# Kernel tuning notes

Hardware: AMD Instinct MI355X
Metric: run time of the kernel (lower is better)

Reference implementation:

```python
import jax, jax.numpy as jnp
import numpy as np

H = 1024   # hidden_size
A = 16     # num_actions
T = 64     # time steps
N = 128    # batch (parallel envs)


def setup_inputs() -> dict:
    key = jax.random.key(0)
    ks = jax.random.split(key, 16)
    s = 0.02  # small-ish init scale for weights
    a_idx = jax.random.randint(ks[5], (T, N), 0, A)
    return {
        "x": jax.random.normal(ks[0], (T * N, H), jnp.float32),
        "hxs_gru": jax.random.normal(ks[1], (N, H), jnp.float32),
        "hxs_p": jax.random.normal(ks[2], (N, 2 * H), jnp.float32),
        # masks are 0/1 episode-reset flags
        "masks": jax.random.bernoulli(ks[3], 0.95, (T * N, 1)).astype(jnp.float32),
        "prev_action_one_hot": jax.nn.one_hot(a_idx, A, dtype=jnp.float32),
        "w_ih": jax.random.normal(ks[6], (3 * H, H), jnp.float32) * s,
        "w_hh": jax.random.normal(ks[7], (3 * H, H), jnp.float32) * s,
        "b_ih": jnp.zeros((3 * H,), jnp.float32),
        "b_hh": jnp.zeros((3 * H,), jnp.float32),
        "p_w1": jax.random.normal(ks[8], (2 * H, 2 * H + A), jnp.float32) * s,
        "p_b1": jnp.zeros((2 * H,), jnp.float32),
        "p_w2": jax.random.normal(ks[9], (H, 2 * H), jnp.float32) * s,
        "p_b2": jnp.zeros((H,), jnp.float32),
        "mu_w": jax.random.normal(ks[10], (H, H), jnp.float32) * s,
        "mu_b": jnp.zeros((H,), jnp.float32),
        "lv_w": jax.random.normal(ks[11], (H, H), jnp.float32) * s,
        "lv_b": jnp.zeros((H,), jnp.float32),
    }


def reference(x, hxs_gru, hxs_p, masks, prev_action_one_hot,
              w_ih, w_hh, b_ih, b_hh,
              p_w1, p_b1, p_w2, p_b2,
              mu_w, mu_b, lv_w, lv_b):
    n = hxs_gru.shape[0]
    h_dim = hxs_gru.shape[1]
    t = x.shape[0] // n
    xT = x.reshape(t, n, h_dim)        # [T,N,H]
    mT = masks.reshape(t, n, 1)        # [T,N,1]

    # ---- _forward_gru: masked GRUCell recurrence over time ----
    def gru_step(h, inp):
        x_t, m_t = inp
        h0 = h * m_t                                  # per-step state reset
        gi = x_t @ w_ih.T + b_ih                      # [N,3H]
        gh = h0 @ w_hh.T + b_hh                       # [N,3H]
        ir, iz, inn = jnp.split(gi, 3, axis=1)
        hr, hz, hn = jnp.split(gh, 3, axis=1)
        r = jax.nn.sigmoid(ir + hr)
        z = jax.nn.sigmoid(iz + hz)
        nn_ = jnp.tanh(inn + r * hn)
        h_new = (1.0 - z) * nn_ + z * h0              # PyTorch GRUCell update
        return h_new, h_new

    gru_hxs, gru_acc = jax.lax.scan(gru_step, hxs_gru, (xT, mT))
    gru_acc = gru_acc.reshape(t * n, h_dim)

    # ---- _forward_p_gru: MLP recurrence with mask-gated state/action ----
    def p_step(h, inp):
        x_t, m_t, a_t = inp
        hidden = h * m_t + jnp.concatenate([x_t, x_t], axis=1) * (1.0 - m_t)
        cur = jnp.concatenate([a_t * m_t, hidden], axis=1)   # [N, A+2H]
        d = jax.nn.relu(cur @ p_w1.T + p_b1)                 # [N, 2H]
        d = jax.nn.relu(d @ p_w2.T + p_b2)                   # [N, H]
        mu = d @ mu_w.T + mu_b                               # [N, H]
        lv = d @ lv_w.T + lv_b                               # [N, H]
        h_new = jnp.concatenate([mu, x_t], axis=1)           # [N, 2H]
        return h_new, (mu, lv)

    # note: original concatenates action first: cat((a*m, hidden))
    p_hxs, (p_mu, p_lv) = jax.lax.scan(p_step, hxs_p, (xT, mT, prev_action_one_hot))
    p_mu = p_mu.reshape(t * n, h_dim)
    p_lv = p_lv.reshape(t * n, h_dim)
    return (gru_acc, gru_hxs, p_mu, p_lv, p_hxs)
```

## Files before the change

### kernel.cpp

```cpp
#include <hip/hip_runtime.h>

typedef unsigned int uint;
typedef unsigned short ushort;
typedef __bf16 bf16x8_t __attribute__((ext_vector_type(8)));
typedef float f32x4_t __attribute__((ext_vector_type(4)));
typedef uint u32x4_t __attribute__((ext_vector_type(4)));

__device__ __forceinline__ ushort f2b(float f) {
    uint u = __builtin_bit_cast(uint, f);
    u += 0x7fffu + ((u >> 16) & 1u);
    return (ushort)(u >> 16);
}
__device__ __forceinline__ float b2f(ushort h) {
    return __builtin_bit_cast(float, (uint)h << 16);
}
__device__ __forceinline__ float sigm(float v) { return 1.f / (1.f + __expf(-v)); }
__device__ __forceinline__ float tanh_(float v) {
    v = fmaxf(-15.f, fminf(15.f, v));
    float e = __expf(2.f * v);
    return (e - 1.f) / (e + 1.f);
}

__device__ __forceinline__ uint ld_cg_u32(const uint* p) {
    uint r;
    asm volatile("global_load_dword %0, %1, off sc0 sc1\n\ts_waitcnt vmcnt(0)"
                 : "=v"(r) : "v"(p) : "memory");
    return r;
}
__device__ __forceinline__ void st_cg_u32(uint* p, uint v) {
    asm volatile("global_store_dword %0, %1, off sc0 sc1" :: "v"(p), "v"(v) : "memory");
}
__device__ __forceinline__ void st_cg_u16(ushort* p, uint v) {
    asm volatile("global_store_short %0, %1, off sc0 sc1" :: "v"(p), "v"(v) : "memory");
}
__device__ __forceinline__ void st_cg_x4(ushort* p, u32x4_t v) {
    asm volatile("global_store_dwordx4 %0, %1, off sc0 sc1" :: "v"(p), "v"(v) : "memory");
}
__device__ __forceinline__ void ld8_nc(uint4 u[8],
    const void* p0, const void* p1, const void* p2, const void* p3,
    const void* p4, const void* p5, const void* p6, const void* p7)
{
    asm volatile(
        "global_load_dwordx4 %0, %8, off\n\t"
        "global_load_dwordx4 %1, %9, off\n\t"
        "global_load_dwordx4 %2, %10, off\n\t"
        "global_load_dwordx4 %3, %11, off\n\t"
        "global_load_dwordx4 %4, %12, off\n\t"
        "global_load_dwordx4 %5, %13, off\n\t"
        "global_load_dwordx4 %6, %14, off\n\t"
        "global_load_dwordx4 %7, %15, off"
        : "=&v"(u[0]), "=&v"(u[1]), "=&v"(u[2]), "=&v"(u[3]),
          "=&v"(u[4]), "=&v"(u[5]), "=&v"(u[6]), "=&v"(u[7])
        : "v"(p0), "v"(p1), "v"(p2), "v"(p3), "v"(p4), "v"(p5), "v"(p6), "v"(p7)
        : "memory");
}
__device__ __forceinline__ void vm0() {
    asm volatile("s_waitcnt vmcnt(0)" ::: "memory");
    __builtin_amdgcn_sched_barrier(0);
}
__device__ __forceinline__ bf16x8_t u2b(uint4 u) { return __builtin_bit_cast(bf16x8_t, u); }

#define SMEM_BYTES 36864
union U8 { ushort h[8]; uint4 v; };

template<int BN, int EPI, bool AF32>
__device__ __forceinline__ void gemm_body(
    int bx, int by, const void* Av, int lda,
    const ushort* Bp, int ldb, int K,
    void* Ov, int ldo, const float* bias, char* smem)
{
    constexpr int LDW = 72;
    ushort* As = (ushort*)smem;
    ushort* Bs = (ushort*)(smem + 128 * LDW * 2);
    const int tid = threadIdx.x, lane = tid & 63, wid = tid >> 6;
    constexpr int WC = (BN == 128) ? 2 : 1;
    constexpr int WR = 4 / WC;
    constexpr int WROWS = 128 / WR;
    constexpr int WCOLS = BN / WC;
    constexpr int MI = WROWS / 16, NI = WCOLS / 16;
    const int wr = (WC == 2) ? (wid >> 1) : wid;
    const int wc = (WC == 2) ? (wid & 1) : 0;
    const int row0 = by * 128, col0 = bx * BN;

    f32x4_t acc[MI][NI];
#pragma unroll
    for (int i = 0; i < MI; i++)
#pragma unroll
        for (int j = 0; j < NI; j++) acc[i][j] = (f32x4_t){0.f, 0.f, 0.f, 0.f};

    for (int k0 = 0; k0 < K; k0 += 64) {
        __syncthreads();
#pragma unroll
        for (int cc = 0; cc < 4; cc++) {
            int chunk = tid + cc * 256;
            int r = chunk >> 3, c8 = chunk & 7;
            uint4 val;
            if constexpr (AF32) {
                const float* Af = (const float*)Av + (size_t)(row0 + r) * lda + k0 + c8 * 8;
                float4 v0 = ((const float4*)Af)[0];
                float4 v1 = ((const float4*)Af)[1];
                U8 u;
                u.h[0] = f2b(v0.x); u.h[1] = f2b(v0.y); u.h[2] = f2b(v0.z); u.h[3] = f2b(v0.w);
                u.h[4] = f2b(v1.x); u.h[5] = f2b(v1.y); u.h[6] = f2b(v1.z); u.h[7] = f2b(v1.w);
                val = u.v;
            } else {
                val = *(const uint4*)((const ushort*)Av + (size_t)(row0 + r) * lda + k0 + c8 * 8);
            }
            *(uint4*)&As[r * LDW + c8 * 8] = val;
        }
#pragma unroll
        for (int cc = 0; cc < BN / 32; cc++) {
            int chunk = tid + cc * 256;
            int r = chunk >> 3, c8 = chunk & 7;
            uint4 val = *(const uint4*)(Bp + (size_t)(col0 + r) * ldb + k0 + c8 * 8);
            *(uint4*)&Bs[r * LDW + c8 * 8] = val;
        }
        __syncthreads();
#pragma unroll
        for (int kk = 0; kk < 64; kk += 32) {
            int ko = kk + ((lane >> 4) << 3);
            bf16x8_t af[MI], bf[NI];
#pragma unroll
            for (int mi = 0; mi < MI; mi++)
                af[mi] = *(const bf16x8_t*)&As[(wr * WROWS + mi * 16 + (lane & 15)) * LDW + ko];
#pragma unroll
            for (int ni = 0; ni < NI; ni++)
                bf[ni] = *(const bf16x8_t*)&Bs[(wc * WCOLS + ni * 16 + (lane & 15)) * LDW + ko];
#pragma unroll
            for (int mi = 0; mi < MI; mi++)
#pragma unroll
                for (int ni = 0; ni < NI; ni++)
                    acc[mi][ni] = __builtin_amdgcn_mfma_f32_16x16x32_bf16(af[mi], bf[ni], acc[mi][ni], 0, 0, 0);
        }
    }
#pragma unroll
    for (int mi = 0; mi < MI; mi++) {
#pragma unroll
        for (int ni = 0; ni < NI; ni++) {
            int gcol = col0 + wc * WCOLS + ni * 16 + (lane & 15);
#pragma unroll
            for (int i = 0; i < 4; i++) {
                int grow = row0 + wr * WROWS + mi * 16 + ((lane >> 4) << 2) + i;
                float v = acc[mi][ni][i];
                if constexpr (EPI == 0) {
                    ((float*)Ov)[(size_t)grow * ldo + gcol] = v + bias[gcol];
                } else if constexpr (EPI == 1) {
                    ((ushort*)Ov)[(size_t)grow * ldo + gcol] = f2b(v);
                } else if constexpr (EPI == 2) {
                    ((ushort*)Ov)[(size_t)grow * ldo + gcol] = f2b(v + bias[gcol]);
                } else if constexpr (EPI == 3) {
                    int t = grow >> 7, row = grow & 127;
                    int g = gcol >> 10, cb = (gcol & 1023) >> 4, c16 = gcol & 15;
                    ((ushort*)Ov)[(((size_t)t * 3 + g) * 64 + cb) * 2048 + row * 16 + c16] = f2b(v);
                } else {
                    int t = grow >> 7, row = grow & 127;
                    int cg = gcol >> 5, c32 = gcol & 31;
                    ((ushort*)Ov)[((size_t)t * 64 + cg) * 4096 + row * 32 + c32] = f2b(v + bias[gcol]);
                }
            }
        }
    }
}

template<int BN, int EPI, bool AF32>
__global__ __launch_bounds__(256) void gemm_k(
    const void* A, int lda, const ushort* B, int ldb, int K,
    void* O, int ldo, const float* bias)
{
    __shared__ char smem[SMEM_BYTES];
    gemm_body<BN, EPI, AF32>(blockIdx.x, blockIdx.y, A, lda, B, ldb, K, O, ldo, bias, smem);
}

__global__ __launch_bounds__(256) void gemm_rest_k(
    const void* A1, const ushort* B1, void* O1,
    const void* A2, const ushort* B2, void* O2,
    const float* p_w1, const float* mu_b, float* cvec)
{
    __shared__ char smem[SMEM_BYTES];
    int b = blockIdx.x;
    if (b < 1536) {
        gemm_body<128, 3, true>(b % 24, b / 24, A1, 1024, B1, 1024, 1024, O1, 0, nullptr, smem);
    } else if (b < 1664) {
        int c = b - 1536;
        gemm_body<128, 1, false>(c & 7, c >> 3, A2, 1024, B2, 1024, 1024, O2, 1024, nullptr, smem);
    } else {
        int j = (b - 1664) * 4 + (threadIdx.x >> 6);
        int lane = threadIdx.x & 63;
        float s = 0.f;
        for (int o = lane; o < 1024; o += 64) s += p_w1[(size_t)j * 2064 + 16 + o] * mu_b[o];
#pragma unroll
        for (int off = 32; off; off >>= 1) s += __shfl_down(s, off);
        if (lane == 0) cvec[j] = s;
    }
}

#define NFLAG_G 0
#define NFLAG_A 4096
#define NFLAG_B 12288
#define NFLAGS  20480

__device__ __forceinline__ void wv_wait16(uint* f, int lane) {
    if (lane < 16) {
        while (ld_cg_u32(f + lane) == 0u) {}
    }
    __builtin_amdgcn_sched_barrier(0);
}
__device__ __forceinline__ void wg_arrive(uint* slot, int tid) {
    __syncthreads();
    if (tid == 0) st_cg_u32(slot, 1u);
}

__device__ void role_gru(int cb, const ushort* __restrict__ whhb, ushort* hb,
                         const ushort* __restrict__ gi, const float* masks,
                         const float* b_ih, const float* b_hh, const float* hxs_g,
                         float* out, uint* flags, char* lds)
{
    const int tid = threadIdx.x, lane = tid & 63, w = tid >> 6;
    const int colL = cb * 16 + (lane & 15);
    const int kw = w * 256;
    const int kl = (lane >> 4) << 3;

    bf16x8_t bw[3][8];
#pragma unroll
    for (int g = 0; g < 3; g++)
#pragma unroll
        for (int ks = 0; ks < 8; ks++)
            bw[g][ks] = *(const bf16x8_t*)(whhb + (size_t)(g * 1024 + colL) * 1024 + kw + ks * 32 + kl);

    const float bihr = b_ih[colL], bihz = b_ih[1024 + colL], bihn = b_ih[2048 + colL];
    const float bhhr = b_hh[colL], bhhz = b_hh[1024 + colL], bhhn = b_hh[2048 + colL];

    f32x4_t hown[2];
#pragma unroll
    for (int j = 0; j < 2; j++)
#pragma unroll
        for (int i = 0; i < 4; i++)
            hown[j][i] = hxs_g[(size_t)((2 * w + j) * 16 + ((lane >> 4) << 2) + i) * 1024 + colL];

    for (int t = 0; t < 64; t++) {
        float mc[2][4], mn[2][4], g0p[2][4], g1p[2][4], g2p[2][4];
        const size_t gb = ((size_t)t * 3 * 64 + cb) * 2048;
#pragma unroll
        for (int j = 0; j < 2; j++) {
            const int rt = 2 * w + j;
#pragma unroll
            for (int i = 0; i < 4; i++) {
                const int row = rt * 16 + ((lane >> 4) << 2) + i;
                mc[j][i] = masks[t * 128 + row];
                mn[j][i] = (t < 63) ? masks[(t + 1) * 128 + row] : 0.f;
                g0p[j][i] = b2f(gi[gb + row * 16 + (lane & 15)]);
                g1p[j][i] = b2f(gi[gb + 131072 + row * 16 + (lane & 15)]);
                g2p[j][i] = b2f(gi[gb + 262144 + row * 16 + (lane & 15)]);
            }
        }
        if (t) wv_wait16(flags + NFLAG_G + (t - 1) * 64 + w * 16, lane);
        const ushort* base = hb + (size_t)t * 131072 + (size_t)(lane & 15) * 1024 + kw + kl;
        f32x4_t acc[3][8];
#pragma unroll
        for (int g = 0; g < 3; g++)
#pragma unroll
            for (int rt = 0; rt < 8; rt++) acc[g][rt] = (f32x4_t){0.f, 0.f, 0.f, 0.f};
#pragma unroll
        for (int half = 0; half < 2; half++) {
            const ushort* b = base + half * 128;
            uint4 u0[8], u1[8], u2[8], u3[8];
            ld8_nc(u0, b, b + 16384, b + 32768, b + 49152, b + 65536, b + 81920, b + 98304, b + 114688);
            ld8_nc(u1, b + 32, b + 16384 + 32, b + 32768 + 32, b + 49152 + 32, b + 65536 + 32, b + 81920 + 32, b + 98304 + 32, b + 114688 + 32);
            ld8_nc(u2, b + 64, b + 16384 + 64, b + 32768 + 64, b + 49152 + 64, b + 65536 + 64, b + 81920 + 64, b + 98304 + 64, b + 114688 + 64);
            ld8_nc(u3, b + 96, b + 16384 + 96, b + 32768 + 96, b + 49152 + 96, b + 65536 + 96, b + 81920 + 96, b + 98304 + 96, b + 114688 + 96);
            vm0();
#pragma unroll
            for (int g = 0; g < 3; g++)
#pragma unroll
                for (int rt = 0; rt < 8; rt++) {
                    acc[g][rt] = __builtin_amdgcn_mfma_f32_16x16x32_bf16(u2b(u0[rt]), bw[g][half * 4 + 0], acc[g][rt], 0, 0, 0);
                    acc[g][rt] = __builtin_amdgcn_mfma_f32_16x16x32_bf16(u2b(u1[rt]), bw[g][half * 4 + 1], acc[g][rt], 0, 0, 0);
                    acc[g][rt] = __builtin_amdgcn_mfma_f32_16x16x32_bf16(u2b(u2[rt]), bw[g][half * 4 + 2], acc[g][rt], 0, 0, 0);
                    acc[g][rt] = __builtin_amdgcn_mfma_f32_16x16x32_bf16(u2b(u3[rt]), bw[g][half * 4 + 3], acc[g][rt], 0, 0, 0);
                }
        }
        __syncthreads();
#pragma unroll
        for (int g = 0; g < 3; g++)
#pragma unroll
            for (int rt = 0; rt < 8; rt++)
                *(f32x4_t*)(lds + ((size_t)(w * 24 + g * 8 + rt) * 64 + lane) * 16) = acc[g][rt];
        __syncthreads();
#pragma unroll
        for (int j = 0; j < 2; j++) {
            const int rt = 2 * w + j;
            f32x4_t sg[3];
#pragma unroll
            for (int g = 0; g < 3; g++) {
                sg[g] = (f32x4_t){0.f, 0.f, 0.f, 0.f};
#pragma unroll
                for (int ww = 0; ww < 4; ww++)
                    sg[g] += *(const f32x4_t*)(lds + ((size_t)(ww * 24 + g * 8 + rt) * 64 + lane) * 16);
            }
#pragma unroll
            for (int i = 0; i < 4; i++) {
                const int row = rt * 16 + ((lane >> 4) << 2) + i;
                const float h0 = hown[j][i] * mc[j][i];
                const float rv = sigm(g0p[j][i] + bihr + bhhr + sg[0][i]);
                const float zv = sigm(g1p[j][i] + bihz + bhhz + sg[1][i]);
                const float nv = tanh_(g2p[j][i] + bihn + rv * (sg[2][i] + bhhn));
                const float hnew = (1.f - zv) * nv + zv * h0;
                out[(size_t)(t * 128 + row) * 1024 + colL] = hnew;
                hown[j][i] = hnew;
                if (t < 63)
                    st_cg_u16(hb + (size_t)(t + 1) * 131072 + (size_t)row * 1024 + colL,
                              (uint)f2b(hnew * mn[j][i]));
            }
        }
        wg_arrive(flags + NFLAG_G + t * 64 + cb, tid);
    }
}

__device__ void role_p(int p, const ushort* __restrict__ Wcb, const ushort* __restrict__ w1h1b,
                       const ushort* __restrict__ hp1b, const ushort* __restrict__ w2b,
                       const ushort* __restrict__ d1pre, const float* masks, const float* cvec,
                       const float* p_b2, ushort* d1r, ushort* d2r, uint* flags, char* lds)
{
    const int tid = threadIdx.x, lane = tid & 63, w = tid >> 6;
    const int rowg = p >> 6, colg = p & 63;
    const int rA0 = rowg * 64, cA0 = colg * 32;
    const int rB0 = rowg * 64, cB0 = colg * 16;
    const int kwA = w * 256, kwB = w * 512, kl = (lane >> 4) << 3;
    ushort* stg = (ushort*)(lds + 32768) + w * 512;

    bf16x8_t wcF[2][8];
#pragma unroll
    for (int ct = 0; ct < 2; ct++)
#pragma unroll
        for (int ks = 0; ks < 8; ks++)
            wcF[ct][ks] = *(const bf16x8_t*)(Wcb + (size_t)(cA0 + ct * 16 + (lane & 15)) * 1024 + kwA + ks * 32 + kl);
    bf16x8_t w2F[16];
#pragma unroll
    for (int ks = 0; ks < 16; ks++)
        w2F[ks] = *(const bf16x8_t*)(w2b + (size_t)(cB0 + (lane & 15)) * 2048 + kwB + ks * 32 + kl);
    const float cv0 = cvec[cA0 + (lane & 15)], cv1 = cvec[cA0 + 16 + (lane & 15)];
    const float pb = p_b2[cB0 + (lane & 15)];

    for (int t = 0; t < 64; t++) {
        float mA[4], preA[2][4];
        const size_t pbase = ((size_t)t * 64 + colg) * 4096;
#pragma unroll
        for (int i = 0; i < 4; i++) {
            const int row = rA0 + w * 16 + ((lane >> 4) << 2) + i;
            mA[i] = masks[t * 128 + row];
            preA[0][i] = b2f(d1pre[pbase + (row & 127) * 32 + (lane & 15)]);
            preA[1][i] = b2f(d1pre[pbase + (row & 127) * 32 + 16 + (lane & 15)]);
        }
        if (t) wv_wait16(flags + NFLAG_B + (t - 1) * 128 + rowg * 64 + w * 16, lane);
        f32x4_t accA[2][4];
#pragma unroll
        for (int ct = 0; ct < 2; ct++)
#pragma unroll
            for (int rt = 0; rt < 4; rt++) accA[ct][rt] = (f32x4_t){0.f, 0.f, 0.f, 0.f};
        if (t == 0) {
#pragma unroll
            for (int ks = 0; ks < 8; ks++) {
                bf16x8_t af[4], b0[2];
#pragma unroll
                for (int ct = 0; ct < 2; ct++)
                    b0[ct] = *(const bf16x8_t*)(w1h1b + (size_t)(cA0 + ct * 16 + (lane & 15)) * 1024 + kwA + ks * 32 + kl);
#pragma unroll
                for (int rt = 0; rt < 4; rt++)
                    af[rt] = *(const bf16x8_t*)(hp1b + (size_t)(rA0 + rt * 16 + (lane & 15)) * 1024 + kwA + ks * 32 + kl);
#pragma unroll
                for (int ct = 0; ct < 2; ct++)
#pragma unroll
                    for (int rt = 0; rt < 4; rt++)
                        accA[ct][rt] = __builtin_amdgcn_mfma_f32_16x16x32_bf16(af[rt], b0[ct], accA[ct][rt], 0, 0, 0);
            }
        } else {
            const ushort* Ab = d2r + (size_t)(t - 1) * 131072 + (size_t)(rA0 + (lane & 15)) * 1024 + kwA + kl;
            uint4 u0[8], u1[8], u2[8], u3[8];
            ld8_nc(u0, Ab,       Ab + 16384,       Ab + 32768,       Ab + 49152,       Ab + 32,  Ab + 16384 + 32,  Ab + 32768 + 32,  Ab + 49152 + 32);
            ld8_nc(u1, Ab + 64,  Ab + 16384 + 64,  Ab + 32768 + 64,  Ab + 49152 + 64,  Ab + 96,  Ab + 16384 + 96,  Ab + 32768 + 96,  Ab + 49152 + 96);
            ld8_nc(u2, Ab + 128, Ab + 16384 + 128, Ab + 32768 + 128, Ab + 49152 + 128, Ab + 160, Ab + 16384 + 160, Ab + 32768 + 160, Ab + 49152 + 160);
            ld8_nc(u3, Ab + 192, Ab + 16384 + 192, Ab + 32768 + 192, Ab + 49152 + 192, Ab + 224, Ab + 16384 + 224, Ab + 32768 + 224, Ab + 49152 + 224);
            vm0();
#pragma unroll
            for (int ct = 0; ct < 2; ct++)
#pragma unroll
                for (int rt = 0; rt < 4; rt++) {
                    accA[ct][rt] = __builtin_amdgcn_mfma_f32_16x16x32_bf16(u2b(u0[rt]), wcF[ct][0], accA[ct][rt], 0, 0, 0);
                    accA[ct][rt] = __builtin_amdgcn_mfma_f32_16x16x32_bf16(u2b(u0[4 + rt]), wcF[ct][1], accA[ct][rt], 0, 0, 0);
                    accA[ct][rt] = __builtin_amdgcn_mfma_f32_16x16x32_bf16(u2b(u1[rt]), wcF[ct][2], accA[ct][rt], 0, 0, 0);
                    accA[ct][rt] = __builtin_amdgcn_mfma_f32_16x16x32_bf16(u2b(u1[4 + rt]), wcF[ct][3], accA[ct][rt], 0, 0, 0);
                    accA[ct][rt] = __builtin_amdgcn_mfma_f32_16x16x32_bf16(u2b(u2[rt]), wcF[ct][4], accA[ct][rt], 0, 0, 0);
                    accA[ct][rt] = __builtin_amdgcn_mfma_f32_16x16x32_bf16(u2b(u2[4 + rt]), wcF[ct][5], accA[ct][rt], 0, 0, 0);
                    accA[ct][rt] = __builtin_amdgcn_mfma_f32_16x16x32_bf16(u2b(u3[rt]), wcF[ct][6], accA[ct][rt], 0, 0, 0);
                    accA[ct][rt] = __builtin_amdgcn_mfma_f32_16x16x32_bf16(u2b(u3[4 + rt]), wcF[ct][7], accA[ct][rt], 0, 0, 0);
                }
        }
        __syncthreads();
#pragma unroll
        for (int ct = 0; ct < 2; ct++)
#pragma unroll
            for (int rt = 0; rt < 4; rt++)
                *(f32x4_t*)(lds + ((size_t)(w * 8 + ct * 4 + rt) * 64 + lane) * 16) = accA[ct][rt];
        __syncthreads();
#pragma unroll
        for (int ct = 0; ct < 2; ct++) {
            f32x4_t s = (f32x4_t){0.f, 0.f, 0.f, 0.f};
#pragma unroll
            for (int ww = 0; ww < 4; ww++)
                s += *(const f32x4_t*)(lds + ((size_t)(ww * 8 + ct * 4 + w) * 64 + lane) * 16);
            const float cvt = (t == 0) ? 0.f : (ct ? cv1 : cv0);
#pragma unroll
            for (int i = 0; i < 4; i++) {
                float f = preA[ct][i] + mA[i] * (s[i] + cvt);
                stg[(((lane >> 4) << 2) + i) * 32 + ct * 16 + (lane & 15)] = f2b(f > 0.f ? f : 0.f);
            }
        }
        __syncthreads();
        {
            const int rl = lane >> 2, c8 = (lane & 3) * 8;
            u32x4_t v = *(const u32x4_t*)&stg[rl * 32 + c8];
            st_cg_x4(d1r + (size_t)t * 262144 + (size_t)(rA0 + w * 16 + rl) * 2048 + cA0 + c8, v);
        }
        wg_arrive(flags + NFLAG_A + t * 128 + p, tid);
        wv_wait16(flags + NFLAG_A + t * 128 + rowg * 64 + w * 16, lane);
        f32x4_t accB[4];
#pragma unroll
        for (int rt = 0; rt < 4; rt++) accB[rt] = (f32x4_t){0.f, 0.f, 0.f, 0.f};
        const ushort* Bb = d1r + (size_t)t * 262144 + (size_t)(rB0 + (lane & 15)) * 2048 + kwB + kl;
#pragma unroll
        for (int half = 0; half < 2; half++) {
            const ushort* b = Bb + half * 256;
            uint4 u0[8], u1[8], u2[8], u3[8];
            ld8_nc(u0, b,       b + 32768,       b + 65536,       b + 98304,       b + 32,  b + 32768 + 32,  b + 65536 + 32,  b + 98304 + 32);
            ld8_nc(u1, b + 64,  b + 32768 + 64,  b + 65536 + 64,  b + 98304 + 64,  b + 96,  b + 32768 + 96,  b + 65536 + 96,  b + 98304 + 96);
            ld8_nc(u2, b + 128, b + 32768 + 128, b + 65536 + 128, b + 98304 + 128, b + 160, b + 32768 + 160, b + 65536 + 160, b + 98304 + 160);
            ld8_nc(u3, b + 192, b + 32768 + 192, b + 65536 + 192, b + 98304 + 192, b + 224, b + 32768 + 224, b + 65536 + 224, b + 98304 + 224);
            vm0();
#pragma unroll
            for (int rt = 0; rt < 4; rt++) {
                accB[rt] = __builtin_amdgcn_mfma_f32_16x16x32_bf16(u2b(u0[rt]), w2F[half * 8 + 0], accB[rt], 0, 0, 0);
                accB[rt] = __builtin_amdgcn_mfma_f32_16x16x32_bf16(u2b(u0[4 + rt]), w2F[half * 8 + 1], accB[rt], 0, 0, 0);
                accB[rt] = __builtin_amdgcn_mfma_f32_16x16x32_bf16(u2b(u1[rt]), w2F[half * 8 + 2], accB[rt], 0, 0, 0);
                accB[rt] = __builtin_amdgcn_mfma_f32_16x16x32_bf16(u2b(u1[4 + rt]), w2F[half * 8 + 3], accB[rt], 0, 0, 0);
                accB[rt] = __builtin_amdgcn_mfma_f32_16x16x32_bf16(u2b(u2[rt]), w2F[half * 8 + 4], accB[rt], 0, 0, 0);
                accB[rt] = __builtin_amdgcn_mfma_f32_16x16x32_bf16(u2b(u2[4 + rt]), w2F[half * 8 + 5], accB[rt], 0, 0, 0);
                accB[rt] = __builtin_amdgcn_mfma_f32_16x16x32_bf16(u2b(u3[rt]), w2F[half * 8 + 6], accB[rt], 0, 0, 0);
                accB[rt] = __builtin_amdgcn_mfma_f32_16x16x32_bf16(u2b(u3[4 + rt]), w2F[half * 8 + 7], accB[rt], 0, 0, 0);
            }
        }
        __syncthreads();
#pragma unroll
        for (int rt = 0; rt < 4; rt++)
            *(f32x4_t*)(lds + ((size_t)(w * 4 + rt) * 64 + lane) * 16) = accB[rt];
        __syncthreads();
        {
            f32x4_t s = (f32x4_t){0.f, 0.f, 0.f, 0.f};
#pragma unroll
            for (int ww = 0; ww < 4; ww++)
                s += *(const f32x4_t*)(lds + ((size_t)(ww * 4 + w) * 64 + lane) * 16);
#pragma unroll
            for (int i = 0; i < 4; i++) {
                float f = s[i] + pb;
                stg[(((lane >> 4) << 2) + i) * 16 + (lane & 15)] = f2b(f > 0.f ? f : 0.f);
            }
        }
        __syncthreads();
        {
            if (lane < 32) {
                const int rl = lane >> 1, c8 = (lane & 1) * 8;
                u32x4_t v = *(const u32x4_t*)&stg[rl * 16 + c8];
                st_cg_x4(d2r + (size_t)t * 131072 + (size_t)(rB0 + w * 16 + rl) * 1024 + cB0 + c8, v);
            }
        }
        wg_arrive(flags + NFLAG_B + t * 128 + p, tid);
    }
}

__global__ __launch_bounds__(256, 1) void persist_k(
    const ushort* whhb, const ushort* Wcb, const ushort* w1h1b, const ushort* w2b,
    const ushort* gi, const ushort* d1pre, const ushort* hp1b,
    ushort* hb, ushort* d1r, ushort* d2r,
    const float* masks, const float* b_ih, const float* b_hh,
    const float* cvec, const float* p_b2, const float* hxs_g,
    float* out, uint* flags)
{
    __shared__ __align__(16) char lds[98304];
    const int wg = blockIdx.x;
    if (wg < 64) role_gru(wg, whhb, hb, gi, masks, b_ih, b_hh, hxs_g, out, flags, lds);
    else         role_p(wg - 64, Wcb, w1h1b, hp1b, w2b, d1pre, masks, cvec, p_b2, d1r, d2r, flags, lds);
}

__global__ void prep_all(const float* w_ih, const float* w_hh, const float* p_w1,
                         const float* p_w2, const float* mu_w, const float* lv_w,
                         const float* x, const float* hxs_g, const float* hxs_p,
                         const float* masks, const float* oh,
                         ushort* wihb, ushort* whhb, ushort* w2b, ushort* muwb,
                         ushort* lvwb, ushort* muwTb, ushort* w1h1b, ushort* pw1b,
                         ushort* ain, ushort* hb0, ushort* hp1b, uint* flags)
{
    const long totW = 17956864;
    const long totA = 8192L * 2112, totH = 131072, totP = 131072;
    const long total = totW + totA + totH + totP + NFLAGS;
    for (long idx = (long)blockIdx.x * 256 + threadIdx.x; idx < total; idx += (long)gridDim.x * 256) {
        long l = idx;
        if (l < 3145728) { wihb[l] = f2b(w_ih[l]); continue; } l -= 3145728;
        if (l < 3145728) { whhb[l] = f2b(w_hh[l]); continue; } l -= 3145728;
        if (l < 2097152) { w2b[l] = f2b(p_w2[l]); continue; } l -= 2097152;
        if (l < 1048576) { muwb[l] = f2b(mu_w[l]); continue; } l -= 1048576;
        if (l < 1048576) { lvwb[l] = f2b(lv_w[l]); continue; } l -= 1048576;
        if (l < 1048576) {
            int c = (int)(l >> 10), o = (int)(l & 1023);
            muwTb[l] = f2b(mu_w[(size_t)o * 1024 + c]); continue;
        } l -= 1048576;
        if (l < 2097152) {
            int r = (int)(l >> 10), c = (int)(l & 1023);
            w1h1b[l] = f2b(p_w1[(size_t)r * 2064 + 16 + c]); continue;
        } l -= 2097152;
        if (l < 4325376) {
            int r = (int)(l / 2112), c = (int)(l - (long)r * 2112);
            pw1b[l] = (c < 2064) ? f2b(p_w1[(size_t)r * 2064 + c]) : (ushort)0;
            continue;
        } l -= 4325376;
        if (l < totA) {
            int i = (int)(l / 2112);
            int c = (int)(l - (long)i * 2112);
            float m = masks[i];
            float v;
            if (c < 16) v = oh[(size_t)i * 16 + c] * m;
            else if (c < 1040) v = x[(size_t)i * 1024 + (c - 16)] * (1.f - m);
            else if (c < 2064) {
                int cc = c - 1040;
                float xp = (i >= 128) ? x[(size_t)(i - 128) * 1024 + cc]
                                      : hxs_p[(size_t)i * 2048 + 1024 + cc];
                v = xp * m + x[(size_t)i * 1024 + cc] * (1.f - m);
            } else v = 0.f;
            ain[l] = f2b(v);
            continue;
        } l -= totA;
        if (l < totH) {
            int row = (int)(l >> 10), c = (int)(l & 1023);
            hb0[l] = f2b(hxs_g[(size_t)row * 1024 + c] * masks[row]);
            continue;
        } l -= totH;
        if (l < totP) {
            int row = (int)(l >> 10), c = (int)(l & 1023);
            hp1b[l] = f2b(hxs_p[(size_t)row * 2048 + c]);
            continue;
        } l -= totP;
        flags[l] = 0u;
    }
}

__global__ void k_tail(float* out, const float* x)
{
    const long total = 131072 + 262144;
    for (long idx = (long)blockIdx.x * 256 + threadIdx.x; idx < total; idx += (long)gridDim.x * 256) {
        if (idx < 131072) {
            out[8388608 + idx] = out[8257536 + idx];
        } else {
            long j = idx - 131072;
            int n = (int)(j >> 11), c = (int)(j & 2047);
            out[25296896 + j] = (c < 1024)
                ? out[8519680 + (size_t)(8064 + n) * 1024 + c]
                : x[(size_t)(8064 + n) * 1024 + (c - 1024)];
        }
    }
}

extern "C" void kernel_launch(void* const* d_in, const int* in_sizes, int n_in,
                              void* d_out, int out_size, void* d_ws, size_t ws_size,
                              hipStream_t stream)
{
    (void)in_sizes; (void)n_in; (void)out_size; (void)ws_size;
    const float* x      = (const float*)d_in[0];
    const float* hxs_g  = (const float*)d_in[1];
    const float* hxs_p  = (const float*)d_in[2];
    const float* masks  = (const float*)d_in[3];
    const float* oh     = (const float*)d_in[4];
    const float* w_ih   = (const float*)d_in[5];
    const float* w_hh   = (const float*)d_in[6];
    const float* b_ih   = (const float*)d_in[7];
    const float* b_hh   = (const float*)d_in[8];
    const float* p_w1   = (const float*)d_in[9];
    const float* p_b1   = (const float*)d_in[10];
    const float* p_w2   = (const float*)d_in[11];
    const float* p_b2   = (const float*)d_in[12];
    const float* mu_w   = (const float*)d_in[13];
    const float* mu_b   = (const float*)d_in[14];
    const float* lv_w   = (const float*)d_in[15];
    const float* lv_b   = (const float*)d_in[16];
    float* out = (float*)d_out;

    char* w = (char*)d_ws;
    ushort* gi     = (ushort*)(w + 0);
    ushort* ain    = (ushort*)(w + 0);
    ushort* d1pre  = (ushort*)(w + 50331648);
    ushort* wihb   = (ushort*)(w + 83886080);
    ushort* whhb   = (ushort*)(w + 90177536);
    ushort* pw1b   = (ushort*)(w + 96468992);
    ushort* w1h1b  = (ushort*)(w + 105119744);
    ushort* w2b    = (ushort*)(w + 109314048);
    ushort* muwb   = (ushort*)(w + 113508352);
    ushort* muwTb  = (ushort*)(w + 115605504);
    ushort* lvwb   = (ushort*)(w + 117702656);
    ushort* Wcb    = (ushort*)(w + 119799808);
    ushort* hp1b   = (ushort*)(w + 123994112);
    ushort* hb     = (ushort*)(w + 124256256);
    ushort* d1r    = (ushort*)(w + 141033472);
    ushort* d2r    = (ushort*)(w + 174587904);
    float*  cvec   = (float*) (w + 191365120);
    uint*   flags  = (uint*)  (w + 191373312);

    prep_all<<<dim3(6144), 256, 0, stream>>>(
        w_ih, w_hh, p_w1, p_w2, mu_w, lv_w, x, hxs_g, hxs_p, masks, oh,
        wihb, whhb, w2b, muwb, lvwb, muwTb, w1h1b, pw1b, ain, hb, hp1b, flags);

    gemm_k<128, 4, false><<<dim3(16, 64), 256, 0, stream>>>(
        ain, 2112, pw1b, 2112, 2112, d1pre, 0, p_b1);
    gemm_rest_k<<<dim3(2176), 256, 0, stream>>>(
        x, wihb, gi, w1h1b, muwTb, Wcb, p_w1, mu_b, cvec);

    persist_k<<<dim3(192), 256, 0, stream>>>(
        whhb, Wcb, w1h1b, w2b, gi, d1pre, hp1b, hb, d1r, d2r,
        masks, b_ih, b_hh, cvec, p_b2, hxs_g, out, flags);

    gemm_k<128, 0, false><<<dim3(8, 64), 256, 0, stream>>>(
        d2r, 1024, muwb, 1024, 1024, out + 8519680, 1024, mu_b);
    gemm_k<128, 0, false><<<dim3(8, 64), 256, 0, stream>>>(
        d2r, 1024, lvwb, 1024, 1024, out + 16908288, 1024, lv_b);

    k_tail<<<dim3(1536), 256, 0, stream>>>(out, x);
}
```

Before: 1.452 ms.

## Merge mu/logvar GEMMs into one launch and use workgroup-wide flag waits

The separate mu and logvar output GEMMs become a single launch over a concatenated weight matrix (lvwb is moved to sit right after muwb). A new epilogue routes columns below 1024 to the mu output and the rest to the logvar output, each with its own bias. In the persistent kernel, the per-wave 16-flag spin waits are replaced by a workgroup-wide wait: 64 threads poll with s_sleep, then a __syncthreads. This is meant to cut launch overhead and spin-polling memory traffic, at the cost of extra barriers on the recurrence's critical path.

```diff
diff --git a/kernel.cpp b/kernel.cpp
--- a/kernel.cpp
+++ b/kernel.cpp
@@ -67,7 +67,7 @@
 __device__ __forceinline__ void gemm_body(
     int bx, int by, const void* Av, int lda,
     const ushort* Bp, int ldb, int K,
-    void* Ov, int ldo, const float* bias, char* smem)
+    void* Ov, int ldo, const float* bias, const float* bias2, char* smem)
 {
     constexpr int LDW = 72;
     ushort* As = (ushort*)smem;
@@ -152,10 +152,15 @@
                     int t = grow >> 7, row = grow & 127;
                     int g = gcol >> 10, cb = (gcol & 1023) >> 4, c16 = gcol & 15;
                     ((ushort*)Ov)[(((size_t)t * 3 + g) * 64 + cb) * 2048 + row * 16 + c16] = f2b(v);
-                } else {
+                } else if constexpr (EPI == 4) {
                     int t = grow >> 7, row = grow & 127;
                     int cg = gcol >> 5, c32 = gcol & 31;
                     ((ushort*)Ov)[((size_t)t * 64 + cg) * 4096 + row * 32 + c32] = f2b(v + bias[gcol]);
+                } else {
+                    if (gcol < 1024)
+                        ((float*)Ov)[8519680 + (size_t)grow * 1024 + gcol] = v + bias[gcol];
+                    else
+                        ((float*)Ov)[16908288 + (size_t)grow * 1024 + (gcol - 1024)] = v + bias2[gcol - 1024];
                 }
             }
         }
@@ -165,10 +170,10 @@
 template<int BN, int EPI, bool AF32>
 __global__ __launch_bounds__(256) void gemm_k(
     const void* A, int lda, const ushort* B, int ldb, int K,
-    void* O, int ldo, const float* bias)
+    void* O, int ldo, const float* bias, const float* bias2)
 {
     __shared__ char smem[SMEM_BYTES];
-    gemm_body<BN, EPI, AF32>(blockIdx.x, blockIdx.y, A, lda, B, ldb, K, O, ldo, bias, smem);
+    gemm_body<BN, EPI, AF32>(blockIdx.x, blockIdx.y, A, lda, B, ldb, K, O, ldo, bias, bias2, smem);
 }
 
 __global__ __launch_bounds__(256) void gemm_rest_k(
@@ -179,10 +184,10 @@
     __shared__ char smem[SMEM_BYTES];
     int b = blockIdx.x;
     if (b < 1536) {
-        gemm_body<128, 3, true>(b % 24, b / 24, A1, 1024, B1, 1024, 1024, O1, 0, nullptr, smem);
+        gemm_body<128, 3, true>(b % 24, b / 24, A1, 1024, B1, 1024, 1024, O1, 0, nullptr, nullptr, smem);
     } else if (b < 1664) {
         int c = b - 1536;
-        gemm_body<128, 1, false>(c & 7, c >> 3, A2, 1024, B2, 1024, 1024, O2, 1024, nullptr, smem);
+        gemm_body<128, 1, false>(c & 7, c >> 3, A2, 1024, B2, 1024, 1024, O2, 1024, nullptr, nullptr, smem);
     } else {
         int j = (b - 1664) * 4 + (threadIdx.x >> 6);
         int lane = threadIdx.x & 63;
@@ -199,11 +204,11 @@
 #define NFLAG_B 12288
 #define NFLAGS  20480
 
-__device__ __forceinline__ void wv_wait16(uint* f, int lane) {
-    if (lane < 16) {
-        while (ld_cg_u32(f + lane) == 0u) {}
-    }
-    __builtin_amdgcn_sched_barrier(0);
+__device__ __forceinline__ void wg_wait(uint* f, int n, int tid) {
+    if (tid < n) {
+        while (ld_cg_u32(f + tid) == 0u) __builtin_amdgcn_s_sleep(1);
+    }
+    __syncthreads();
 }
 __device__ __forceinline__ void wg_arrive(uint* slot, int tid) {
     __syncthreads();
@@ -253,7 +258,7 @@
                 g2p[j][i] = b2f(gi[gb + 262144 + row * 16 + (lane & 15)]);
             }
         }
-        if (t) wv_wait16(flags + NFLAG_G + (t - 1) * 64 + w * 16, lane);
+        if (t) wg_wait(flags + NFLAG_G + (t - 1) * 64, 64, tid);
         const ushort* base = hb + (size_t)t * 131072 + (size_t)(lane & 15) * 1024 + kw + kl;
         f32x4_t acc[3][8];
 #pragma unroll
@@ -351,7 +356,7 @@
             preA[0][i] = b2f(d1pre[pbase + (row & 127) * 32 + (lane & 15)]);
             preA[1][i] = b2f(d1pre[pbase + (row & 127) * 32 + 16 + (lane & 15)]);
         }
-        if (t) wv_wait16(flags + NFLAG_B + (t - 1) * 128 + rowg * 64 + w * 16, lane);
+        if (t) wg_wait(flags + NFLAG_B + (t - 1) * 128 + rowg * 64, 64, tid);
         f32x4_t accA[2][4];
 #pragma unroll
         for (int ct = 0; ct < 2; ct++)
@@ -422,7 +427,7 @@
             st_cg_x4(d1r + (size_t)t * 262144 + (size_t)(rA0 + w * 16 + rl) * 2048 + cA0 + c8, v);
         }
         wg_arrive(flags + NFLAG_A + t * 128 + p, tid);
-        wv_wait16(flags + NFLAG_A + t * 128 + rowg * 64 + w * 16, lane);
+        wg_wait(flags + NFLAG_A + t * 128 + rowg * 64, 64, tid);
         f32x4_t accB[4];
 #pragma unroll
         for (int rt = 0; rt < 4; rt++) accB[rt] = (f32x4_t){0.f, 0.f, 0.f, 0.f};
@@ -601,8 +606,8 @@
     ushort* w1h1b  = (ushort*)(w + 105119744);
     ushort* w2b    = (ushort*)(w + 109314048);
     ushort* muwb   = (ushort*)(w + 113508352);
-    ushort* muwTb  = (ushort*)(w + 115605504);
-    ushort* lvwb   = (ushort*)(w + 117702656);
+    ushort* lvwb   = (ushort*)(w + 115605504);
+    ushort* muwTb  = (ushort*)(w + 117702656);
     ushort* Wcb    = (ushort*)(w + 119799808);
     ushort* hp1b   = (ushort*)(w + 123994112);
     ushort* hb     = (ushort*)(w + 124256256);
@@ -616,7 +621,7 @@
         wihb, whhb, w2b, muwb, lvwb, muwTb, w1h1b, pw1b, ain, hb, hp1b, flags);
 
     gemm_k<128, 4, false><<<dim3(16, 64), 256, 0, stream>>>(
-        ain, 2112, pw1b, 2112, 2112, d1pre, 0, p_b1);
+        ain, 2112, pw1b, 2112, 2112, d1pre, 0, p_b1, nullptr);
     gemm_rest_k<<<dim3(2176), 256, 0, stream>>>(
         x, wihb, gi, w1h1b, muwTb, Wcb, p_w1, mu_b, cvec);
 
@@ -624,10 +629,8 @@
         whhb, Wcb, w1h1b, w2b, gi, d1pre, hp1b, hb, d1r, d2r,
         masks, b_ih, b_hh, cvec, p_b2, hxs_g, out, flags);
 
-    gemm_k<128, 0, false><<<dim3(8, 64), 256, 0, stream>>>(
-        d2r, 1024, muwb, 1024, 1024, out + 8519680, 1024, mu_b);
-    gemm_k<128, 0, false><<<dim3(8, 64), 256, 0, stream>>>(
-        d2r, 1024, lvwb, 1024, 1024, out + 16908288, 1024, lv_b);
+    gemm_k<128, 5, false><<<dim3(16, 64), 256, 0, stream>>>(
+        d2r, 1024, muwb, 1024, 1024, out, 0, mu_b, lv_b);
 
     k_tail<<<dim3(1536), 256, 0, stream>>>(out, x);
 }
```

Result: faster. 1.414 ms (median of 2 runs) (-2.7%).
